# Optimization experiments

Hardware: AMD Instinct MI355X
Metric: run time of the kernel (lower is better)

## Reference

```python
import jax, jax.numpy as jnp
import numpy as np

D_MODEL = 192; D_INNER = 384; N_STATE = 16; D_CONV = 4; DT_RANK = 12; DEPTH = 24
PATCH = 16; STRIDE = 16; IMG = 128; EPS = 1e-5


def _ln(x, w, b):
    m = jnp.mean(x, -1, keepdims=True)
    v = jnp.mean((x - m) ** 2, -1, keepdims=True)
    return (x - m) * jax.lax.rsqrt(v + EPS) * w + b


def _mamba_dir(xz, cw, cb, xpw, dpw, dpb, Alog, Dv):
    # xz: (B, L, 2*d_inner); one direction of the bidirectional Mamba mixer
    xp, z = jnp.split(xz, 2, axis=-1)               # (B,L,di) each
    xc = jnp.transpose(xp, (0, 2, 1))               # (B,di,L)
    xc = jnp.pad(xc, ((0, 0), (0, 0), (D_CONV - 1, 0)))  # causal pad
    xc = jax.lax.conv_general_dilated(
        xc, cw, (1,), 'VALID',
        dimension_numbers=('NCH', 'OIH', 'NCH'),
        feature_group_count=D_INNER) + cb[None, :, None]
    u = jax.nn.silu(jnp.transpose(xc, (0, 2, 1)))   # (B,L,di)
    dbl = u @ xpw.T                                  # (B,L,dt_rank+2N)
    dt, Bm, Cm = jnp.split(dbl, [DT_RANK, DT_RANK + N_STATE], axis=-1)
    dt = jax.nn.softplus(dt @ dpw.T + dpb)           # (B,L,di)
    A = -jnp.exp(Alog)                               # (di,N)
    dA = jnp.exp(dt[..., None] * A)                  # (B,L,di,N)
    dBu = (dt * u)[..., None] * Bm[:, :, None, :]    # (B,L,di,N)

    def comb(c1, c2):
        a1, b1 = c1
        a2, b2 = c2
        return a1 * a2, a2 * b1 + b2

    _, h = jax.lax.associative_scan(comb, (dA, dBu), axis=1)
    y = jnp.einsum('bldn,bln->bld', h, Cm) + u * Dv
    return y * jax.nn.silu(z)


def _forward(x, patch_w, patch_b, ln_w, ln_b, in_w,
             cf_w, cf_b, xpf_w, dtf_w, dtf_b, Alog_f, D_f,
             cbk_w, cbk_b, xpb_w, dtb_w, dtb_b, Alog_b, D_b,
             out_w, nf_w, nf_b, head_w, head_b):
    B = x.shape[0]
    p = jax.lax.conv_general_dilated(
        x, patch_w, (STRIDE,) * 3, 'VALID',
        dimension_numbers=('NCDHW', 'OIDHW', 'NCDHW')) + patch_b[None, :, None, None, None]
    hidden = p.reshape(B, D_MODEL, -1).transpose(0, 2, 1)  # (B, L=512, D)
    residual = jnp.zeros_like(hidden)

    xs = (ln_w, ln_b, in_w, cf_w, cf_b, xpf_w, dtf_w, dtf_b, Alog_f, D_f,
          cbk_w, cbk_b, xpb_w, dtb_w, dtb_b, Alog_b, D_b, out_w)

    def step(carry, pl):
        hidden, residual = carry
        (lw, lb, iw, cfw, cfb, xpf, dwf, dbf, Af, Dfv,
         cbw, cbb, xpb, dwb, dbb, Ab, Dbv, ow) = pl
        residual = residual + hidden
        hn = _ln(residual, lw, lb)
        xz = hn @ iw.T                               # (B,L,2di)
        yf = _mamba_dir(xz, cfw, cfb, xpf, dwf, dbf, Af, Dfv)
        yb = jnp.flip(_mamba_dir(jnp.flip(xz, 1), cbw, cbb, xpb, dwb, dbb, Ab, Dbv), 1)
        hidden = (yf + yb) @ ow.T
        return (hidden, residual), None

    (hidden, residual), _ = jax.lax.scan(step, (hidden, residual), xs)
    final = _ln(residual + hidden, nf_w, nf_b)
    feat = final[:, -1, :]                           # final_pool_type='none' -> last token
    return feat @ head_w.T + head_b


def setup_inputs() -> dict:
    key = jax.random.key(0)
    ks = jax.random.split(key, 16)
    rn = lambda k, s, sc=0.02: jax.random.normal(k, s, jnp.float32) * sc
    d = {}
    d['x'] = jax.random.normal(ks[0], (1, 1, IMG, IMG, IMG), jnp.float32)
    d['patch_w'] = rn(ks[1], (D_MODEL, 1, PATCH, PATCH, PATCH), 0.05)
    d['patch_b'] = jnp.zeros((D_MODEL,), jnp.float32)
    d['ln_w'] = jnp.ones((DEPTH, D_MODEL), jnp.float32)
    d['ln_b'] = jnp.zeros((DEPTH, D_MODEL), jnp.float32)
    d['in_w'] = rn(ks[2], (DEPTH, 2 * D_INNER, D_MODEL))
    d['cf_w'] = rn(ks[3], (DEPTH, D_INNER, 1, D_CONV), 0.2)
    d['cf_b'] = jnp.zeros((DEPTH, D_INNER), jnp.float32)
    d['xpf_w'] = rn(ks[4], (DEPTH, DT_RANK + 2 * N_STATE, D_INNER))
    d['dtf_w'] = rn(ks[5], (DEPTH, D_INNER, DT_RANK), 0.1)
    d['dtf_b'] = jnp.full((DEPTH, D_INNER), -4.6, jnp.float32)  # softplus -> dt~0.01
    d['Alog_f'] = jnp.log(jnp.broadcast_to(jnp.arange(1, N_STATE + 1, dtype=jnp.float32), (DEPTH, D_INNER, N_STATE)))
    d['D_f'] = jnp.ones((DEPTH, D_INNER), jnp.float32)
    d['cbk_w'] = rn(ks[6], (DEPTH, D_INNER, 1, D_CONV), 0.2)
    d['cbk_b'] = jnp.zeros((DEPTH, D_INNER), jnp.float32)
    d['xpb_w'] = rn(ks[7], (DEPTH, DT_RANK + 2 * N_STATE, D_INNER))
    d['dtb_w'] = rn(ks[8], (DEPTH, D_INNER, DT_RANK), 0.1)
    d['dtb_b'] = jnp.full((DEPTH, D_INNER), -4.6, jnp.float32)
    d['Alog_b'] = jnp.log(jnp.broadcast_to(jnp.arange(1, N_STATE + 1, dtype=jnp.float32), (DEPTH, D_INNER, N_STATE)))
    d['D_b'] = jnp.ones((DEPTH, D_INNER), jnp.float32)
    d['out_w'] = rn(ks[9], (DEPTH, D_MODEL, D_INNER))
    d['nf_w'] = jnp.ones((D_MODEL,), jnp.float32)
    d['nf_b'] = jnp.zeros((D_MODEL,), jnp.float32)
    d['head_w'] = rn(ks[10], (2, D_MODEL))
    d['head_b'] = jnp.zeros((2,), jnp.float32)
    return d


def reference(x, patch_w, patch_b, ln_w, ln_b, in_w,
              cf_w, cf_b, xpf_w, dtf_w, dtf_b, Alog_f, D_f,
              cbk_w, cbk_b, xpb_w, dtb_w, dtb_b, Alog_b, D_b,
              out_w, nf_w, nf_b, head_w, head_b):
    return _forward(x, patch_w, patch_b, ln_w, ln_b, in_w,
                    cf_w, cf_b, xpf_w, dtf_w, dtf_b, Alog_f, D_f,
                    cbk_w, cbk_b, xpb_w, dtb_w, dtb_b, Alog_b, D_b,
                    out_w, nf_w, nf_b, head_w, head_b)
```

## Files before the change

kernel.cpp:

```cpp
#include <hip/hip_runtime.h>
#include <hip/hip_bf16.h>

#define D_MODEL 192
#define D_INNER 384
#define N_STATE 16
#define DT_RANK 12
#define DEPTH 24
#define SEQ 512
#define NCHUNK 8
#define CLEN 64
#define TS 68
#define AS 33
#define PART_STRIDE (SEQ * D_MODEL)
#define USTR (SEQ * D_INNER)
#define KSPLIT 16

typedef __hip_bfloat16 bf16;
typedef unsigned short u16;

__device__ __forceinline__ float silu_f(float x) { return x / (1.f + __expf(-x)); }
__device__ __forceinline__ float softplus_f(float x) {
    return (x > 20.f) ? x : log1pf(__expf(x));
}
__device__ __forceinline__ float bf2f(unsigned u) {
    return __uint_as_float(u << 16);
}
__device__ __forceinline__ u16 f2bu(float f) {
    bf16 b = __float2bfloat16(f);
    return *reinterpret_cast<u16*>(&b);
}

template<typename T> __device__ __forceinline__ float ld(const void* p, long i) {
    return ((const float*)p)[i];
}
template<> __device__ __forceinline__ float ld<bf16>(const void* p, long i) {
    return bf2f(((const u16*)p)[i]);
}
template<typename T> __device__ __forceinline__ float4 ld4(const void* p, long i) {
    return *(const float4*)((const float*)p + i);
}
template<> __device__ __forceinline__ float4 ld4<bf16>(const void* p, long i) {
    const ushort4 v = *(const ushort4*)((const u16*)p + i);
    return make_float4(bf2f(v.x), bf2f(v.y), bf2f(v.z), bf2f(v.w));
}
template<typename T> __device__ __forceinline__ void st(void* p, int i, float v) {
    ((float*)p)[i] = v;
}
template<> __device__ __forceinline__ void st<bf16>(void* p, int i, float v) {
    ((bf16*)p)[i] = __float2bfloat16(v);
}
__device__ __forceinline__ float dot4(const float4& a, const float4& b) {
    return a.x * b.x + a.y * b.y + a.z * b.z + a.w * b.w;
}
__device__ __forceinline__ void ld8b(const u16* p, float4& a, float4& b) {
    const uint4 u = *(const uint4*)p;
    a.x = bf2f(u.x & 0xffffu); a.y = bf2f(u.x >> 16);
    a.z = bf2f(u.y & 0xffffu); a.w = bf2f(u.y >> 16);
    b.x = bf2f(u.z & 0xffffu); b.y = bf2f(u.z >> 16);
    b.z = bf2f(u.w & 0xffffu); b.w = bf2f(u.w >> 16);
}
__device__ __forceinline__ float4 ld4b(const u16* p) {
    const uint2 u = *(const uint2*)p;
    return make_float4(bf2f(u.x & 0xffffu), bf2f(u.x >> 16),
                       bf2f(u.y & 0xffffu), bf2f(u.y >> 16));
}

struct Prep {
    const void *inw, *ow, *xpwf, *xpwb, *dtwf, *dtwb, *cwf, *cwb,
               *lnw, *lnb, *cbf, *cbb, *dtbf, *dtbb, *Af, *Ab, *Df, *Db,
               *x, *pw, *pb;
    u16 *inwB, *owB, *xpwfB, *xpwbB, *dtwfB, *dtwbB, *cwfB, *cwbB, *xB, *pwB;
    float *lnwF, *lnbF, *cbfF, *cbbF, *dtbfF, *dtbbF, *negAfF, *negAbF, *DfF, *DbF, *pbF;
    int* flag;
};
__device__ void cvtB(const void* s, u16* d, long n, long g, long str, int isb) {
    if (isb) {
        const u16* p = (const u16*)s;
        for (long i = g * 4; i < n; i += str * 4) *(ushort4*)(d + i) = *(const ushort4*)(p + i);
    } else {
        const float* p = (const float*)s;
        for (long i = g * 4; i < n; i += str * 4) {
            const float4 v = *(const float4*)(p + i);
            ushort4 o; o.x = f2bu(v.x); o.y = f2bu(v.y); o.z = f2bu(v.z); o.w = f2bu(v.w);
            *(ushort4*)(d + i) = o;
        }
    }
}
__device__ void cvtF(const void* s, float* d, long n, long g, long str, int isb) {
    if (isb) {
        const u16* p = (const u16*)s;
        for (long i = g * 4; i < n; i += str * 4) {
            const ushort4 v = *(const ushort4*)(p + i);
            *(float4*)(d + i) = make_float4(bf2f(v.x), bf2f(v.y), bf2f(v.z), bf2f(v.w));
        }
    } else {
        const float* p = (const float*)s;
        for (long i = g * 4; i < n; i += str * 4) *(float4*)(d + i) = *(const float4*)(p + i);
    }
}
__device__ void cvtNA(const void* s, float* d, long n, long g, long str, int isb) {
    if (isb) {
        const u16* p = (const u16*)s;
        for (long i = g * 4; i < n; i += str * 4) {
            const ushort4 v = *(const ushort4*)(p + i);
            *(float4*)(d + i) = make_float4(-__expf(bf2f(v.x)), -__expf(bf2f(v.y)),
                                            -__expf(bf2f(v.z)), -__expf(bf2f(v.w)));
        }
    } else {
        const float* p = (const float*)s;
        for (long i = g * 4; i < n; i += str * 4) {
            const float4 v = *(const float4*)(p + i);
            *(float4*)(d + i) = make_float4(-__expf(v.x), -__expf(v.y), -__expf(v.z), -__expf(v.w));
        }
    }
}
__global__ void __launch_bounds__(256) prep_kernel(Prep a) {
    const long g = (long)blockIdx.x * 256 + threadIdx.x;
    const long str = (long)gridDim.x * 256;
    const int isb = (((const unsigned*)a.lnw)[0] != 0x3F800000u);
    if (g == 0) *a.flag = isb;
    cvtB(a.inw,  a.inwB,  3538944, g, str, isb);
    cvtB(a.ow,   a.owB,   1769472, g, str, isb);
    cvtB(a.x,    a.xB,    2097152, g, str, isb);
    cvtB(a.pw,   a.pwB,    786432, g, str, isb);
    cvtB(a.xpwf, a.xpwfB,  405504, g, str, isb);
    cvtB(a.xpwb, a.xpwbB,  405504, g, str, isb);
    cvtB(a.dtwf, a.dtwfB,  110592, g, str, isb);
    cvtB(a.dtwb, a.dtwbB,  110592, g, str, isb);
    cvtB(a.cwf,  a.cwfB,    36864, g, str, isb);
    cvtB(a.cwb,  a.cwbB,    36864, g, str, isb);
    cvtF(a.lnw,  a.lnwF,     4608, g, str, isb);
    cvtF(a.lnb,  a.lnbF,     4608, g, str, isb);
    cvtF(a.cbf,  a.cbfF,     9216, g, str, isb);
    cvtF(a.cbb,  a.cbbF,     9216, g, str, isb);
    cvtF(a.dtbf, a.dtbfF,    9216, g, str, isb);
    cvtF(a.dtbb, a.dtbbF,    9216, g, str, isb);
    cvtF(a.pb,   a.pbF,       192, g, str, isb);
    cvtNA(a.Af,  a.negAfF,  147456, g, str, isb);
    cvtNA(a.Ab,  a.negAbF,  147456, g, str, isb);
    cvtF(a.Df,   a.DfF,      9216, g, str, isb);
    cvtF(a.Db,   a.DbF,      9216, g, str, isb);
}

__global__ void __launch_bounds__(256) patch_kernel(const u16* xB, const u16* pwB,
                                                    const float* pbF, float* hidC) {
    __shared__ float As_[32 * AS];
    __shared__ float Ws[32 * TS];
    const int mt = blockIdx.x, nt = blockIdx.y, ks = blockIdx.z;
    const int m0 = mt * 32, n0 = nt * 64, kk0 = ks * 256;
    const int tid = threadIdx.x, ty = tid >> 4, tx = tid & 15;
    float acc[2][4] = {};
    for (int kk = kk0; kk < kk0 + 256; kk += 32) {
        for (int e = tid; e < 1024; e += 256) {
            const int m = e >> 5, k = e & 31;
            const int kid = kk + k, t = m0 + m;
            const int dz = kid >> 8, dy = (kid >> 4) & 15, dx = kid & 15;
            const int pz = t >> 6, py = (t >> 3) & 7, px = t & 7;
            As_[k * AS + m] = bf2f(xB[(long)(pz * 16 + dz) * 16384 + (py * 16 + dy) * 128 + (px * 16 + dx)]);
        }
        for (int e = tid; e < 2048; e += 256) {
            const int n = e >> 5, k = e & 31;
            Ws[k * TS + n] = bf2f(pwB[(long)(n0 + n) * 4096 + kk + k]);
        }
        __syncthreads();
        #pragma unroll 8
        for (int k = 0; k < 32; ++k) {
            const float a0 = As_[k * AS + ty * 2];
            const float a1 = As_[k * AS + ty * 2 + 1];
            const float4 w4 = *(const float4*)&Ws[k * TS + tx * 4];
            acc[0][0] += a0 * w4.x; acc[0][1] += a0 * w4.y;
            acc[0][2] += a0 * w4.z; acc[0][3] += a0 * w4.w;
            acc[1][0] += a1 * w4.x; acc[1][1] += a1 * w4.y;
            acc[1][2] += a1 * w4.z; acc[1][3] += a1 * w4.w;
        }
        __syncthreads();
    }
    float* C = hidC + (long)ks * PART_STRIDE;
    #pragma unroll
    for (int i = 0; i < 2; ++i) {
        float4 o4 = make_float4(acc[i][0], acc[i][1], acc[i][2], acc[i][3]);
        if (ks == 0) {
            o4.x += pbF[n0 + tx * 4 + 0];
            o4.y += pbF[n0 + tx * 4 + 1];
            o4.z += pbF[n0 + tx * 4 + 2];
            o4.w += pbF[n0 + tx * 4 + 3];
        }
        *(float4*)&C[(m0 + ty * 2 + i) * D_MODEL + n0 + tx * 4] = o4;
    }
}

__global__ void __launch_bounds__(256) fusedA_kernel(int l, int first,
        const float* hidC, const float* y, const float* resIn, float* resOut,
        const float* lnwF, const float* lnbF, const u16* inwB, const u16* owB, float* xz) {
    __shared__ float sy[2 * D_INNER];
    __shared__ float lnS[2 * D_MODEL];
    __shared__ float hnS[2 * D_MODEL];
    const int tid = threadIdx.x;
    const int t0 = blockIdx.x * 2;
    if (!first) {
        for (int i = tid; i < 2 * D_INNER; i += 256) {
            const int tt = i / D_INNER, d = i - tt * D_INNER;
            const long o = (long)(t0 + tt) * D_INNER + d;
            sy[i] = y[o] + y[(long)USTR + o];
        }
    }
    __syncthreads();
    if (tid < D_MODEL) {
        float accB[2];
        if (first) {
            #pragma unroll
            for (int tt = 0; tt < 2; ++tt) {
                float s = 0.f;
                #pragma unroll
                for (int sp = 0; sp < KSPLIT; ++sp)
                    s += hidC[(long)sp * PART_STRIDE + (t0 + tt) * D_MODEL + tid];
                accB[tt] = s;
            }
        } else {
            accB[0] = accB[1] = 0.f;
            const u16* wr = owB + (long)(l - 1) * D_MODEL * D_INNER + (long)tid * D_INNER;
            for (int k = 0; k < D_INNER; k += 8) {
                float4 a, b;
                ld8b(wr + k, a, b);
                accB[0] += dot4(a, *(const float4*)&sy[k]) + dot4(b, *(const float4*)&sy[k + 4]);
                accB[1] += dot4(a, *(const float4*)&sy[D_INNER + k]) + dot4(b, *(const float4*)&sy[D_INNER + k + 4]);
            }
        }
        #pragma unroll
        for (int tt = 0; tt < 2; ++tt) {
            const float rv = accB[tt] + (first ? 0.f : resIn[(t0 + tt) * D_MODEL + tid]);
            lnS[tt * D_MODEL + tid] = rv;
            resOut[(t0 + tt) * D_MODEL + tid] = rv;
        }
    }
    __syncthreads();
    {
        const int w = tid >> 6, lane = tid & 63;
        if (w < 2) {
            const float v0 = lnS[w * D_MODEL + lane];
            const float v1 = lnS[w * D_MODEL + lane + 64];
            const float v2 = lnS[w * D_MODEL + lane + 128];
            float s = v0 + v1 + v2;
            #pragma unroll
            for (int o = 32; o > 0; o >>= 1) s += __shfl_xor(s, o, 64);
            const float mean = s * (1.f / D_MODEL);
            const float d0 = v0 - mean, d1 = v1 - mean, d2 = v2 - mean;
            float s2 = d0 * d0 + d1 * d1 + d2 * d2;
            #pragma unroll
            for (int o = 32; o > 0; o >>= 1) s2 += __shfl_xor(s2, o, 64);
            const float rstd = rsqrtf(s2 * (1.f / D_MODEL) + 1e-5f);
            hnS[w * D_MODEL + lane]       = d0 * rstd * lnwF[l * D_MODEL + lane]       + lnbF[l * D_MODEL + lane];
            hnS[w * D_MODEL + lane + 64]  = d1 * rstd * lnwF[l * D_MODEL + lane + 64]  + lnbF[l * D_MODEL + lane + 64];
            hnS[w * D_MODEL + lane + 128] = d2 * rstd * lnwF[l * D_MODEL + lane + 128] + lnbF[l * D_MODEL + lane + 128];
        }
    }
    __syncthreads();
    float accD[3][2] = {};
    const u16* w0 = inwB + (long)l * 2 * D_INNER * D_MODEL;
    for (int k = 0; k < D_MODEL; k += 8) {
        #pragma unroll
        for (int r = 0; r < 3; ++r) {
            float4 a, b;
            ld8b(w0 + (long)(tid + r * 256) * D_MODEL + k, a, b);
            #pragma unroll
            for (int tt = 0; tt < 2; ++tt) {
                accD[r][tt] += dot4(a, *(const float4*)&hnS[tt * D_MODEL + k])
                             + dot4(b, *(const float4*)&hnS[tt * D_MODEL + k + 4]);
            }
        }
    }
    #pragma unroll
    for (int r = 0; r < 3; ++r)
        #pragma unroll
        for (int tt = 0; tt < 2; ++tt)
            xz[(long)(t0 + tt) * 2 * D_INNER + tid + r * 256] = accD[r][tt];
}

__global__ void __launch_bounds__(256) stage_kernel(int l, const float* xz,
        const u16* cwfB, const float* cbfF, const u16* xpwfB, const u16* dtwfB, const float* dtbfF,
        const u16* cwbB, const float* cbbF, const u16* xpwbB, const u16* dtwbB, const float* dtbbF,
        float* u, float* dbl, float* dt) {
    __shared__ float su[2 * D_INNER];
    __shared__ float dblP[192];
    __shared__ float dblS[96];
    const int dir = blockIdx.y;
    const u16* cwB  = dir ? cwbB  : cwfB;
    const float* cbF = dir ? cbbF : cbfF;
    const u16* xpwB = dir ? xpwbB : xpwfB;
    const u16* dtwB = dir ? dtwbB : dtwfB;
    const float* dtbF = dir ? dtbbF : dtbfF;
    const int tid = threadIdx.x;
    const int t0 = blockIdx.x * 2;
    float* ub = u + (long)dir * USTR;
    for (int i = tid; i < 2 * D_INNER; i += 256) {
        const int tt = i / D_INNER, d = i - tt * D_INNER;
        const int t = t0 + tt;
        const float4 w4 = ld4b(cwB + (long)(l * D_INNER + d) * 4);
        const float cwk[4] = {w4.x, w4.y, w4.z, w4.w};
        float acc = cbF[l * D_INNER + d];
        #pragma unroll
        for (int k = 0; k < 4; ++k) {
            const int ii = t + k - 3;
            if (ii >= 0) {
                const int src = dir ? (511 - ii) : ii;
                acc += xz[(long)src * 2 * D_INNER + d] * cwk[k];
            }
        }
        const float uv = silu_f(acc);
        su[tt * D_INNER + d] = uv;
        ub[(long)t * D_INNER + d] = uv;
    }
    __syncthreads();
    if (tid < 176) {
        const int half = tid / 88;
        const int r = tid - half * 88;
        const int tt = r / 44, out = r - tt * 44;
        const u16* wr = xpwB + (long)(l * 44 + out) * D_INNER;
        const int k0 = half * 192;
        float acc = 0.f;
        for (int k = k0; k < k0 + 192; k += 8) {
            float4 a, b;
            ld8b(wr + k, a, b);
            acc += dot4(a, *(const float4*)&su[tt * D_INNER + k])
                 + dot4(b, *(const float4*)&su[tt * D_INNER + k + 4]);
        }
        dblP[half * 96 + tt * 48 + out] = acc;
    }
    __syncthreads();
    if (tid < 88) {
        const int tt = tid / 44, out = tid - tt * 44;
        const float s = dblP[tt * 48 + out] + dblP[96 + tt * 48 + out];
        dblS[tt * 48 + out] = s;
        dbl[(long)dir * SEQ * 44 + (long)(t0 + tt) * 44 + out] = s;
    }
    __syncthreads();
    float* dtp = dt + (long)dir * USTR;
    for (int i = tid; i < 2 * D_INNER; i += 256) {
        const int tt = i / D_INNER, d = i - tt * D_INNER;
        const u16* wr = dtwB + (long)(l * D_INNER + d) * DT_RANK;
        const float4 wa = ld4b(wr), wb2 = ld4b(wr + 4), wc = ld4b(wr + 8);
        const float* ds = &dblS[tt * 48];
        float acc = dtbF[l * D_INNER + d]
            + wa.x * ds[0] + wa.y * ds[1] + wa.z * ds[2] + wa.w * ds[3]
            + wb2.x * ds[4] + wb2.y * ds[5] + wb2.z * ds[6] + wb2.w * ds[7]
            + wc.x * ds[8] + wc.y * ds[9] + wc.z * ds[10] + wc.w * ds[11];
        dtp[(long)(t0 + tt) * D_INNER + d] = softplus_f(acc);
    }
}

__global__ void __launch_bounds__(256) scan1_kernel(int l, const float* u, const float* dbl,
        const float* dt, const float* negAf, const float* negAb, float* chunkH, float* chunkP) {
    __shared__ float sU[CLEN * 16];
    __shared__ float sDT[CLEN * 16];
    __shared__ float sB[CLEN * 16];
    const int dg = blockIdx.x, chunk = blockIdx.y, dir = blockIdx.z;
    const int tid = threadIdx.x;
    const int ch = tid >> 4, np = tid & 15;
    const int d0 = dg * 16, d = d0 + ch;
    const int t0 = chunk * CLEN;
    const float* ub = u + (long)dir * USTR;
    const float* dtp = dt + (long)dir * USTR;
    const float* db = dbl + (long)dir * SEQ * 44;
    {
        const int t = tid >> 2, dl4 = (tid & 3) * 4;
        const long base = (long)(t0 + t) * D_INNER + d0 + dl4;
        *(float4*)&sU[t * 16 + dl4]  = *(const float4*)&ub[base];
        *(float4*)&sDT[t * 16 + dl4] = *(const float4*)&dtp[base];
        *(float4*)&sB[t * 16 + dl4]  = *(const float4*)&db[(long)(t0 + t) * 44 + DT_RANK + dl4];
    }
    const float* negA = dir ? negAb : negAf;
    const float A = negA[(long)(l * D_INNER + d) * N_STATE + np];
    __syncthreads();
    float h = 0.f, dts = 0.f;
    for (int t = 0; t < CLEN; ++t) {
        const float dtv = sDT[t * 16 + ch];
        h = __expf(dtv * A) * h + (dtv * sU[t * 16 + ch]) * sB[t * 16 + np];
        dts += dtv;
    }
    const long base = ((long)(dir * NCHUNK + chunk) * D_INNER + d) * N_STATE + np;
    chunkH[base] = h;
    chunkP[base] = __expf(A * dts);
}

__global__ void __launch_bounds__(256) scan2_kernel(int l, const float* xz,
        const float* u, const float* dbl, const float* dt,
        const float* negAf, const float* negAb, const float* DfF, const float* DbF,
        const float* chunkH, const float* chunkP, float* y) {
    __shared__ float sU[CLEN * 16];
    __shared__ float sDT[CLEN * 16];
    __shared__ float sBC[CLEN * 32];
    __shared__ float sZ[CLEN * 16];
    __shared__ float sY[CLEN * 16];
    const int dg = blockIdx.x, chunk = blockIdx.y, dir = blockIdx.z;
    const int tid = threadIdx.x;
    const int ch = tid >> 4, np = tid & 15;
    const int d0 = dg * 16, d = d0 + ch;
    const int t0 = chunk * CLEN;
    const float* ub = u + (long)dir * USTR;
    const float* dtp = dt + (long)dir * USTR;
    const float* db = dbl + (long)dir * SEQ * 44;
    float* yb = y + (long)dir * USTR;
    {
        const int t = tid >> 2, dl4 = (tid & 3) * 4;
        const int tg = t0 + t;
        const long base = (long)tg * D_INNER + d0 + dl4;
        *(float4*)&sU[t * 16 + dl4]  = *(const float4*)&ub[base];
        *(float4*)&sDT[t * 16 + dl4] = *(const float4*)&dtp[base];
        const int out_l = dir ? (511 - tg) : tg;
        *(float4*)&sZ[t * 16 + dl4] = *(const float4*)&xz[(long)out_l * 2 * D_INNER + D_INNER + d0 + dl4];
    }
    for (int i = tid; i < 512; i += 256) {
        const int t = i >> 3, j4 = (i & 7) * 4;
        *(float4*)&sBC[t * 32 + j4] = *(const float4*)&db[(long)(t0 + t) * 44 + DT_RANK + j4];
    }
    const float* negA = dir ? negAb : negAf;
    const float* Dp = dir ? DbF : DfF;
    const float A = negA[(long)(l * D_INNER + d) * N_STATE + np];
    const float Dval = Dp[l * D_INNER + d];
    float h = 0.f;
    for (int c = 0; c < chunk; ++c) {
        const long base = ((long)(dir * NCHUNK + c) * D_INNER + d) * N_STATE + np;
        h = chunkP[base] * h + chunkH[base];
    }
    __syncthreads();
    for (int t = 0; t < CLEN; ++t) {
        const float dtv = sDT[t * 16 + ch];
        const float uv = sU[t * 16 + ch];
        h = __expf(dtv * A) * h + (dtv * uv) * sBC[t * 32 + np];
        float part = h * sBC[t * 32 + 16 + np];
        part += __shfl_xor(part, 1, 64);
        part += __shfl_xor(part, 2, 64);
        part += __shfl_xor(part, 4, 64);
        part += __shfl_xor(part, 8, 64);
        if (np == 0)
            sY[t * 16 + ch] = (part + uv * Dval) * silu_f(sZ[t * 16 + ch]);
    }
    __syncthreads();
    {
        const int t = tid >> 2, dl4 = (tid & 3) * 4;
        const int tg = t0 + t;
        const int out_l = dir ? (511 - tg) : tg;
        *(float4*)&yb[(long)out_l * D_INNER + d0 + dl4] = *(const float4*)&sY[t * 16 + dl4];
    }
}

template<typename T>
__device__ void final_body(const float* res, const float* y, const void* ow,
                           const void* nw, const void* nb, const void* hw, const void* hb,
                           void* out, float* syf, float* f, float* red) {
    const int tid = threadIdx.x;
    for (int i = tid; i < D_INNER; i += 192)
        syf[i] = y[(long)511 * D_INNER + i] + y[(long)USTR + 511 * D_INNER + i];
    __syncthreads();
    float acc = 0.f;
    const long wrow = (long)(DEPTH - 1) * D_MODEL * D_INNER + (long)tid * D_INNER;
    for (int k = 0; k < D_INNER; k += 4)
        acc += dot4(ld4<T>(ow, wrow + k), *(const float4*)&syf[k]);
    const float v = res[511 * D_MODEL + tid] + acc;
    float s = v;
    #pragma unroll
    for (int o = 32; o > 0; o >>= 1) s += __shfl_down(s, o, 64);
    if ((tid & 63) == 0) red[tid >> 6] = s;
    __syncthreads();
    const float mean = (red[0] + red[1] + red[2]) * (1.f / D_MODEL);
    const float d = v - mean;
    float s2 = d * d;
    #pragma unroll
    for (int o = 32; o > 0; o >>= 1) s2 += __shfl_down(s2, o, 64);
    if ((tid & 63) == 0) red[3 + (tid >> 6)] = s2;
    __syncthreads();
    const float var = (red[3] + red[4] + red[5]) * (1.f / D_MODEL);
    f[tid] = d * rsqrtf(var + 1e-5f) * ld<T>(nw, tid) + ld<T>(nb, tid);
    __syncthreads();
    if (tid < 2) {
        float a2 = ld<T>(hb, tid);
        for (int c = 0; c < D_MODEL; ++c) a2 += f[c] * ld<T>(hw, tid * D_MODEL + c);
        st<T>(out, tid, a2);
    }
}
__global__ void final_kernel(const int* flag, const float* res, const float* y, const void* ow,
                             const void* nw, const void* nb, const void* hw, const void* hb,
                             void* out) {
    __shared__ float syf[D_INNER];
    __shared__ float f[D_MODEL];
    __shared__ float red[6];
    if (*flag) final_body<bf16>(res, y, ow, nw, nb, hw, hb, out, syf, f, red);
    else       final_body<float>(res, y, ow, nw, nb, hw, hb, out, syf, f, red);
}

extern "C" void kernel_launch(void* const* d_in, const int* in_sizes, int n_in,
                              void* d_out, int out_size, void* d_ws, size_t ws_size,
                              hipStream_t stream) {
    const void* x    = d_in[0];
    const void* pw   = d_in[1];
    const void* pb   = d_in[2];
    const void* lnw  = d_in[3];
    const void* lnb  = d_in[4];
    const void* inw  = d_in[5];
    const void* cfw  = d_in[6];
    const void* cfb  = d_in[7];
    const void* xpfw = d_in[8];
    const void* dtfw = d_in[9];
    const void* dtfb = d_in[10];
    const void* Af   = d_in[11];
    const void* Dfv  = d_in[12];
    const void* cbw  = d_in[13];
    const void* cbb  = d_in[14];
    const void* xpbw = d_in[15];
    const void* dtbw = d_in[16];
    const void* dtbb = d_in[17];
    const void* Ab   = d_in[18];
    const void* Dbv  = d_in[19];
    const void* ow   = d_in[20];
    const void* nfw  = d_in[21];
    const void* nfb  = d_in[22];
    const void* hw   = d_in[23];
    const void* hb   = d_in[24];

    int* flag = (int*)d_ws;
    float* w = (float*)((char*)d_ws + 16);
    float* hidC   = w;  w += KSPLIT * PART_STRIDE;
    float* res0   = w;  w += PART_STRIDE;
    float* res1   = w;  w += PART_STRIDE;
    float* xz     = w;  w += SEQ * 2 * D_INNER;
    float* u      = w;  w += 2 * USTR;
    float* dbl    = w;  w += 2 * SEQ * 44;
    float* dt     = w;  w += 2 * USTR;
    float* y      = w;  w += 2 * USTR;
    float* chunkH = w;  w += 2 * NCHUNK * D_INNER * N_STATE;
    float* chunkP = w;  w += 2 * NCHUNK * D_INNER * N_STATE;
    float* lnwF = w;  w += 4608;
    float* lnbF = w;  w += 4608;
    float* cbfF = w;  w += 9216;
    float* cbbF = w;  w += 9216;
    float* dtbfF = w; w += 9216;
    float* dtbbF = w; w += 9216;
    float* negAfF = w; w += 147456;
    float* negAbF = w; w += 147456;
    float* DfF = w;   w += 9216;
    float* DbF = w;   w += 9216;
    float* pbF = w;   w += 192;
    u16* b = (u16*)w;
    u16* inwB  = b;  b += 3538944;
    u16* owB   = b;  b += 1769472;
    u16* xB    = b;  b += 2097152;
    u16* pwB   = b;  b += 786432;
    u16* xpwfB = b;  b += 405504;
    u16* xpwbB = b;  b += 405504;
    u16* dtwfB = b;  b += 110592;
    u16* dtwbB = b;  b += 110592;
    u16* cwfB  = b;  b += 36864;
    u16* cwbB  = b;  b += 36864;
    float* res[2] = { res0, res1 };

    Prep pa;
    pa.inw = inw; pa.ow = ow; pa.xpwf = xpfw; pa.xpwb = xpbw;
    pa.dtwf = dtfw; pa.dtwb = dtbw; pa.cwf = cfw; pa.cwb = cbw;
    pa.lnw = lnw; pa.lnb = lnb; pa.cbf = cfb; pa.cbb = cbb;
    pa.dtbf = dtfb; pa.dtbb = dtbb; pa.Af = Af; pa.Ab = Ab; pa.Df = Dfv; pa.Db = Dbv;
    pa.x = x; pa.pw = pw; pa.pb = pb;
    pa.inwB = inwB; pa.owB = owB; pa.xpwfB = xpwfB; pa.xpwbB = xpwbB;
    pa.dtwfB = dtwfB; pa.dtwbB = dtwbB; pa.cwfB = cwfB; pa.cwbB = cwbB;
    pa.xB = xB; pa.pwB = pwB;
    pa.lnwF = lnwF; pa.lnbF = lnbF; pa.cbfF = cbfF; pa.cbbF = cbbF;
    pa.dtbfF = dtbfF; pa.dtbbF = dtbbF; pa.negAfF = negAfF; pa.negAbF = negAbF;
    pa.DfF = DfF; pa.DbF = DbF; pa.pbF = pbF; pa.flag = flag;
    prep_kernel<<<1024, 256, 0, stream>>>(pa);

    patch_kernel<<<dim3(16, 3, KSPLIT), 256, 0, stream>>>(xB, pwB, pbF, hidC);

    for (int l = 0; l < DEPTH; ++l) {
        const int first = (l == 0);
        fusedA_kernel<<<256, 256, 0, stream>>>(l, first, hidC, y,
            res[l & 1], res[(l + 1) & 1], lnwF, lnbF, inwB, owB, xz);
        stage_kernel<<<dim3(256, 2), 256, 0, stream>>>(l, xz,
            cwfB, cbfF, xpwfB, dtwfB, dtbfF,
            cwbB, cbbF, xpwbB, dtwbB, dtbbF, u, dbl, dt);
        scan1_kernel<<<dim3(24, NCHUNK, 2), 256, 0, stream>>>(l, u, dbl, dt,
            negAfF, negAbF, chunkH, chunkP);
        scan2_kernel<<<dim3(24, NCHUNK, 2), 256, 0, stream>>>(l, xz, u, dbl, dt,
            negAfF, negAbF, DfF, DbF, chunkH, chunkP, y);
    }

    final_kernel<<<1, 192, 0, stream>>>(flag, res0, y, ow, nfw, nfb, hw, hb, d_out);
}
```

Before: 1.898 ms.

## Merge two-pass chunked scan into one kernel that recomputes prefix state

```diff
diff --git a/kernel.cpp b/kernel.cpp
--- a/kernel.cpp
+++ b/kernel.cpp
@@ -348,44 +348,10 @@
     }
 }
 
-__global__ void __launch_bounds__(256) scan1_kernel(int l, const float* u, const float* dbl,
-        const float* dt, const float* negAf, const float* negAb, float* chunkH, float* chunkP) {
-    __shared__ float sU[CLEN * 16];
-    __shared__ float sDT[CLEN * 16];
-    __shared__ float sB[CLEN * 16];
-    const int dg = blockIdx.x, chunk = blockIdx.y, dir = blockIdx.z;
-    const int tid = threadIdx.x;
-    const int ch = tid >> 4, np = tid & 15;
-    const int d0 = dg * 16, d = d0 + ch;
-    const int t0 = chunk * CLEN;
-    const float* ub = u + (long)dir * USTR;
-    const float* dtp = dt + (long)dir * USTR;
-    const float* db = dbl + (long)dir * SEQ * 44;
-    {
-        const int t = tid >> 2, dl4 = (tid & 3) * 4;
-        const long base = (long)(t0 + t) * D_INNER + d0 + dl4;
-        *(float4*)&sU[t * 16 + dl4]  = *(const float4*)&ub[base];
-        *(float4*)&sDT[t * 16 + dl4] = *(const float4*)&dtp[base];
-        *(float4*)&sB[t * 16 + dl4]  = *(const float4*)&db[(long)(t0 + t) * 44 + DT_RANK + dl4];
-    }
-    const float* negA = dir ? negAb : negAf;
-    const float A = negA[(long)(l * D_INNER + d) * N_STATE + np];
-    __syncthreads();
-    float h = 0.f, dts = 0.f;
-    for (int t = 0; t < CLEN; ++t) {
-        const float dtv = sDT[t * 16 + ch];
-        h = __expf(dtv * A) * h + (dtv * sU[t * 16 + ch]) * sB[t * 16 + np];
-        dts += dtv;
-    }
-    const long base = ((long)(dir * NCHUNK + chunk) * D_INNER + d) * N_STATE + np;
-    chunkH[base] = h;
-    chunkP[base] = __expf(A * dts);
-}
-
-__global__ void __launch_bounds__(256) scan2_kernel(int l, const float* xz,
+__global__ void __launch_bounds__(256) scanM_kernel(int l, const float* xz,
         const float* u, const float* dbl, const float* dt,
         const float* negAf, const float* negAb, const float* DfF, const float* DbF,
-        const float* chunkH, const float* chunkP, float* y) {
+        float* y) {
     __shared__ float sU[CLEN * 16];
     __shared__ float sDT[CLEN * 16];
     __shared__ float sBC[CLEN * 32];
@@ -395,32 +361,45 @@
     const int tid = threadIdx.x;
     const int ch = tid >> 4, np = tid & 15;
     const int d0 = dg * 16, d = d0 + ch;
-    const int t0 = chunk * CLEN;
     const float* ub = u + (long)dir * USTR;
     const float* dtp = dt + (long)dir * USTR;
     const float* db = dbl + (long)dir * SEQ * 44;
     float* yb = y + (long)dir * USTR;
-    {
-        const int t = tid >> 2, dl4 = (tid & 3) * 4;
-        const int tg = t0 + t;
-        const long base = (long)tg * D_INNER + d0 + dl4;
-        *(float4*)&sU[t * 16 + dl4]  = *(const float4*)&ub[base];
-        *(float4*)&sDT[t * 16 + dl4] = *(const float4*)&dtp[base];
-        const int out_l = dir ? (511 - tg) : tg;
-        *(float4*)&sZ[t * 16 + dl4] = *(const float4*)&xz[(long)out_l * 2 * D_INNER + D_INNER + d0 + dl4];
-    }
-    for (int i = tid; i < 512; i += 256) {
-        const int t = i >> 3, j4 = (i & 7) * 4;
-        *(float4*)&sBC[t * 32 + j4] = *(const float4*)&db[(long)(t0 + t) * 44 + DT_RANK + j4];
-    }
     const float* negA = dir ? negAb : negAf;
     const float* Dp = dir ? DbF : DfF;
     const float A = negA[(long)(l * D_INNER + d) * N_STATE + np];
     const float Dval = Dp[l * D_INNER + d];
+    const int tload = tid >> 2, l4 = (tid & 3) * 4;
     float h = 0.f;
     for (int c = 0; c < chunk; ++c) {
-        const long base = ((long)(dir * NCHUNK + c) * D_INNER + d) * N_STATE + np;
-        h = chunkP[base] * h + chunkH[base];
+        const int tc = c * CLEN;
+        __syncthreads();
+        {
+            const long base = (long)(tc + tload) * D_INNER + d0 + l4;
+            *(float4*)&sU[tload * 16 + l4]  = *(const float4*)&ub[base];
+            *(float4*)&sDT[tload * 16 + l4] = *(const float4*)&dtp[base];
+            *(float4*)&sBC[tload * 32 + l4] = *(const float4*)&db[(long)(tc + tload) * 44 + DT_RANK + l4];
+        }
+        __syncthreads();
+        #pragma unroll 4
+        for (int t = 0; t < CLEN; ++t) {
+            const float dtv = sDT[t * 16 + ch];
+            h = __expf(dtv * A) * h + (dtv * sU[t * 16 + ch]) * sBC[t * 32 + np];
+        }
+    }
+    const int t0 = chunk * CLEN;
+    __syncthreads();
+    {
+        const int tg = t0 + tload;
+        const long base = (long)tg * D_INNER + d0 + l4;
+        *(float4*)&sU[tload * 16 + l4]  = *(const float4*)&ub[base];
+        *(float4*)&sDT[tload * 16 + l4] = *(const float4*)&dtp[base];
+        const int out_l = dir ? (511 - tg) : tg;
+        *(float4*)&sZ[tload * 16 + l4] = *(const float4*)&xz[(long)out_l * 2 * D_INNER + D_INNER + d0 + l4];
+    }
+    for (int i = tid; i < 512; i += 256) {
+        const int t = i >> 3, j4 = (i & 7) * 4;
+        *(float4*)&sBC[t * 32 + j4] = *(const float4*)&db[(long)(t0 + t) * 44 + DT_RANK + j4];
     }
     __syncthreads();
     for (int t = 0; t < CLEN; ++t) {
@@ -437,10 +416,9 @@
     }
     __syncthreads();
     {
-        const int t = tid >> 2, dl4 = (tid & 3) * 4;
-        const int tg = t0 + t;
+        const int tg = t0 + tload;
         const int out_l = dir ? (511 - tg) : tg;
-        *(float4*)&yb[(long)out_l * D_INNER + d0 + dl4] = *(const float4*)&sY[t * 16 + dl4];
+        *(float4*)&yb[(long)out_l * D_INNER + d0 + l4] = *(const float4*)&sY[tload * 16 + l4];
     }
 }
 
@@ -527,8 +505,6 @@
     float* dbl    = w;  w += 2 * SEQ * 44;
     float* dt     = w;  w += 2 * USTR;
     float* y      = w;  w += 2 * USTR;
-    float* chunkH = w;  w += 2 * NCHUNK * D_INNER * N_STATE;
-    float* chunkP = w;  w += 2 * NCHUNK * D_INNER * N_STATE;
     float* lnwF = w;  w += 4608;
     float* lnbF = w;  w += 4608;
     float* cbfF = w;  w += 9216;
@@ -576,10 +552,8 @@
         stage_kernel<<<dim3(256, 2), 256, 0, stream>>>(l, xz,
             cwfB, cbfF, xpwfB, dtwfB, dtbfF,
             cwbB, cbbF, xpwbB, dtwbB, dtbbF, u, dbl, dt);
-        scan1_kernel<<<dim3(24, NCHUNK, 2), 256, 0, stream>>>(l, u, dbl, dt,
-            negAfF, negAbF, chunkH, chunkP);
-        scan2_kernel<<<dim3(24, NCHUNK, 2), 256, 0, stream>>>(l, xz, u, dbl, dt,
-            negAfF, negAbF, DfF, DbF, chunkH, chunkP, y);
+        scanM_kernel<<<dim3(24, NCHUNK, 2), 256, 0, stream>>>(l, xz, u, dbl, dt,
+            negAfF, negAbF, DfF, DbF, y);
     }
 
     final_kernel<<<1, 192, 0, stream>>>(flag, res0, y, ow, nfw, nfb, hw, hb, d_out);
```

New measurement: 2.162 ms. 13.9% more time.
